# Kernel tuning notes

Measured on AMD Instinct MI355X. Metric: run time of the kernel, lower is better.

## Reference

```python
import jax, jax.numpy as jnp
import numpy as np

B, P, G = 16, 16000, 256          # images, RPN proposals, gt boxes per image
S = 512                           # batch_size_per_image
POS_FRAC = 0.25
FG_T, BG_T = 0.5, 0.5             # fg/bg IoU thresholds
NUM_CLASSES = 91
BOX_W = jnp.array([10.0, 10.0, 5.0, 5.0], jnp.float32)  # box_coder weights
BETA = 1.0 / 9.0                  # smooth_l1 beta


def _make_boxes(k, n, img=800.0, maxwh=200.0):
    k1, k2 = jax.random.split(k)
    xy = jax.random.uniform(k1, (B, n, 2)) * img
    wh = jax.random.uniform(k2, (B, n, 2)) * maxwh + 1.0
    return jnp.concatenate([xy, xy + wh], -1)


def setup_inputs() -> dict:
    key = jax.random.key(0)
    ks = jax.random.split(key, 6)
    proposals = _make_boxes(ks[0], P)
    gt_boxes = _make_boxes(ks[1], G)
    gt_labels = jax.random.randint(ks[2], (B, G), 1, NUM_CLASSES)
    gt_thetas = jax.random.uniform(ks[3], (B, G)) * np.pi
    class_logits = jax.random.normal(ks[4], (B * S, NUM_CLASSES))
    box_regression = jax.random.normal(ks[5], (B * S, NUM_CLASSES * 5))
    return dict(class_logits=class_logits, box_regression=box_regression,
                proposals=proposals, gt_boxes=gt_boxes,
                gt_thetas=gt_thetas, gt_labels=gt_labels)


def _box_iou(a, b):
    # a: [G,4] gt, b: [M,4] proposals -> [G,M]
    area_a = (a[:, 2] - a[:, 0]) * (a[:, 3] - a[:, 1])
    area_b = (b[:, 2] - b[:, 0]) * (b[:, 3] - b[:, 1])
    lt = jnp.maximum(a[:, None, :2], b[None, :, :2])
    rb = jnp.minimum(a[:, None, 2:], b[None, :, 2:])
    wh = jnp.clip(rb - lt, 0.0)
    inter = wh[..., 0] * wh[..., 1]
    return inter / (area_a[:, None] + area_b[None, :] - inter)


def _encode(ref, prop):
    pw = prop[:, 2] - prop[:, 0]; ph = prop[:, 3] - prop[:, 1]
    px = prop[:, 0] + 0.5 * pw;   py = prop[:, 1] + 0.5 * ph
    gw = ref[:, 2] - ref[:, 0];   gh = ref[:, 3] - ref[:, 1]
    gx = ref[:, 0] + 0.5 * gw;    gy = ref[:, 1] + 0.5 * gh
    t = jnp.stack([(gx - px) / pw, (gy - py) / ph,
                   jnp.log(gw / pw), jnp.log(gh / ph)], 1)
    return t * BOX_W[None, :]


def _select_training_samples(props, gtb, gtl, gtt):
    # add_gt_proposals
    props_all = jnp.concatenate([props, gtb], 0)        # [P+G,4]
    # assign_targets_to_proposals (Matcher, allow_low_quality=False)
    iou = _box_iou(gtb, props_all)                      # [G,P+G]
    vals = iou.max(0)
    matches = iou.argmax(0)                             # clamped matched idxs
    below = vals < BG_T
    between = (vals >= BG_T) & (vals < FG_T)
    lbl = gtl[matches]
    lbl = jnp.where(below, 0, lbl)      # background
    lbl = jnp.where(between, -1, lbl)   # ignored
    # BalancedPositiveNegativeSampler (deterministic first-k variant)
    pos = lbl > 0
    neg = lbl == 0
    n_pos = jnp.minimum(pos.sum(), int(S * POS_FRAC))
    sel_pos = pos & (jnp.cumsum(pos) <= n_pos)
    sel_neg = neg & (jnp.cumsum(neg) <= (S - n_pos))
    mask = sel_pos | sel_neg
    sampled = jnp.argsort((~mask).astype(jnp.int32), stable=True)[:S]  # sorted selected idxs
    props_s = props_all[sampled]
    lbl_s = lbl[sampled]
    m = matches[sampled]
    reg = _encode(gtb[m], props_s)                       # [S,4]
    reg_t = jnp.concatenate([reg, gtt[m][:, None]], 1)   # append theta -> [S,5]
    return lbl_s, reg_t


def _fastrcnn_loss(class_logits, box_regression, labels, reg_targets):
    N = class_logits.shape[0]
    logp = jax.nn.log_softmax(class_logits, -1)
    cls_loss = -jnp.take_along_axis(logp, labels[:, None], 1).mean()
    br = box_regression.reshape(N, -1, 5)
    idx = jnp.broadcast_to(labels[:, None, None], (N, 1, 5))
    pred = jnp.take_along_axis(br, idx, axis=1)[:, 0, :]
    d = pred - reg_targets
    ad = jnp.abs(d)
    sl1 = jnp.where(ad < BETA, 0.5 * d * d / BETA, ad - 0.5 * BETA)
    pos = (labels > 0).astype(sl1.dtype)
    box_loss = jnp.sum(sl1 * pos[:, None]) / N
    return jnp.stack([cls_loss, box_loss])


def reference(class_logits, box_regression, proposals, gt_boxes, gt_thetas, gt_labels):
    labels, reg_t = jax.vmap(_select_training_samples)(proposals, gt_boxes, gt_labels, gt_thetas)
    labels = labels.reshape(-1)
    reg_t = reg_t.reshape(-1, 5)
    return _fastrcnn_loss(class_logits, box_regression, labels, reg_t)
```

## Files before the change

kernel.cpp:

```cpp
#include <hip/hip_runtime.h>

#define NB 16
#define NP 16000
#define NG 256
#define NM (NP + NG)
#define NSTRIP 254
#define NS 512
#define NCLS 91
#define SL1_BETA (1.0f/9.0f)
#define LOSS_BLOCKS 512

__global__ __launch_bounds__(256) void match_kernel(
    const float4* __restrict__ props4,
    const float4* __restrict__ gt4,
    const int*    __restrict__ gt_labels,
    unsigned long long* __restrict__ posmask,
    unsigned int* __restrict__ posinfo)
{
    __shared__ float4   gbox[NG];
    __shared__ float    gar[NG];
    __shared__ int      glab[NG];
    __shared__ unsigned qm[256][9];

    const int b   = blockIdx.y;
    const int tid = threadIdx.x;

    {
        const float4 v = gt4[(size_t)b * NG + tid];
        gbox[tid] = v;
        gar[tid]  = (v.z - v.x) * (v.w - v.y);
        glab[tid] = gt_labels[b * NG + tid];
    }
    __syncthreads();

    const int j = blockIdx.x * 256 + tid;
    if (j >= NM) return;

    if (j >= NP) {
        int g = j - NP;
        posinfo[(size_t)b * NM + j] = ((unsigned)g << 16) | (unsigned)glab[g];
        if ((tid & 63) == 0) posmask[b * NSTRIP + (j >> 6)] = ~0ull;
        return;
    }

    const float4 p  = props4[(size_t)b * NP + j];
    const float  ap = (p.z - p.x) * (p.w - p.y);

    int qcnt = 0, gfirst = 0;
    for (int w = 0; w < 8; ++w) {
        unsigned m = 0;
        #pragma unroll
        for (int t = 0; t < 32; ++t) {
            const int g = w * 32 + t;
            const float4 gb = gbox[g];
            const float  ga = gar[g];
            float lx = fmaxf(gb.x, p.x), ly = fmaxf(gb.y, p.y);
            float rx = fminf(gb.z, p.z), ry = fminf(gb.w, p.w);
            float ww = fmaxf(rx - lx, 0.0f), hh = fmaxf(ry - ly, 0.0f);
            float inter = ww * hh;
            float tt = ga + ap;
            if (fmaf(inter, 3.0f, -tt) >= 0.0f) m |= (1u << t);
        }
        qm[tid][w] = m;
        if (qcnt == 0 && m) gfirst = w * 32 + (__ffs(m) - 1);
        qcnt += __popc(m);
    }

    const bool pos = qcnt > 0;
    unsigned long long word = __ballot(pos);
    if ((tid & 63) == 0) posmask[b * NSTRIP + (j >> 6)] = word;

    if (pos) {
        int gstar = gfirst;
        if (qcnt > 1) {
            float ib = -1.0f, ub = 1.0f; gstar = 0;
            for (int w = 0; w < 8; ++w) {
                unsigned m = qm[tid][w];
                while (m) {
                    int t = __ffs(m) - 1; m &= m - 1;
                    int g = w * 32 + t;
                    const float4 gb = gbox[g];
                    float lx = fmaxf(gb.x, p.x), ly = fmaxf(gb.y, p.y);
                    float rx = fminf(gb.z, p.z), ry = fminf(gb.w, p.w);
                    float ww = fmaxf(rx - lx, 0.0f), hh = fmaxf(ry - ly, 0.0f);
                    float inter = ww * hh;
                    float u = (gar[g] + ap) - inter;
                    if (inter * ub > ib * u) { ib = inter; ub = u; gstar = g; }
                }
            }
        }
        posinfo[(size_t)b * NM + j] = ((unsigned)gstar << 16) | (unsigned)glab[gstar];
    }
}

__global__ __launch_bounds__(256) void sample_kernel(
    const float4* __restrict__ props4,
    const float4* __restrict__ gt4,
    const float*  __restrict__ gt_thetas,
    const unsigned long long* __restrict__ posmask,
    const unsigned int* __restrict__ posinfo,
    int*   __restrict__ labels_out,
    float* __restrict__ regt_out)
{
    __shared__ int sampled[NS];
    __shared__ int wsum[4];

    const int b    = blockIdx.x;
    const int tid  = threadIdx.x;
    const int lane = tid & 63;
    const int wid  = tid >> 6;

    unsigned long long pm = 0ull, nm = 0ull;
    if (tid < NSTRIP) { pm = posmask[b * NSTRIP + tid]; nm = ~pm; }
    int cp = __popcll(pm), cn = __popcll(nm);
    int val  = (cp << 16) | cn;
    int incl = val;
    #pragma unroll
    for (int off = 1; off < 64; off <<= 1) {
        int u = __shfl_up(incl, off, 64);
        if (lane >= off) incl += u;
    }
    if (lane == 63) wsum[wid] = incl;
    __syncthreads();
    int wbase = 0;
    #pragma unroll
    for (int w = 0; w < 4; ++w) if (w < wid) wbase += wsum[w];
    int tot  = wsum[0] + wsum[1] + wsum[2] + wsum[3];
    int excl = wbase + incl - val;
    int rp = excl >> 16, rn = excl & 0xffff;
    int posT = tot >> 16, negT = tot & 0xffff;
    int np = posT < 128 ? posT : 128;
    int nn = NS - np; if (nn > negT) nn = negT;

    const int base = tid * 64;
    if (tid < NSTRIP) {
        #pragma unroll 4
        for (int e = 0; e < 64; ++e) {
            int idx = base + e;
            if ((pm >> e) & 1ull) {
                if (rp < np) sampled[rp + (rn < nn ? rn : nn)] = idx;
                rp++;
            } else {
                if (rn < nn) sampled[rn + (rp < np ? rp : np)] = idx;
                rn++;
            }
        }
    }
    __syncthreads();
    if (tid == 0 && np + nn < NS) {
        int cpp = 0, cnn = 0, i = np + nn;
        for (int idx = 0; idx < NM && i < NS; ++idx) {
            unsigned long long w = posmask[b * NSTRIP + (idx >> 6)];
            bool p = (w >> (idx & 63)) & 1ull;
            bool sel;
            if (p) { sel = cpp < np; cpp++; } else { sel = cnn < nn; cnn++; }
            if (!sel) sampled[i++] = idx;
        }
    }
    __syncthreads();

    for (int i = tid; i < NS; i += 256) {
        int idx = sampled[i];
        unsigned long long w = posmask[b * NSTRIP + (idx >> 6)];
        bool pos = (w >> (idx & 63)) & 1ull;
        int lbl = 0;
        if (pos) {
            unsigned info = posinfo[(size_t)b * NM + idx];
            int m = info >> 16; lbl = info & 0xffff;
            float4 pv = (idx < NP) ? props4[(size_t)b * NP + idx]
                                   : gt4[(size_t)b * NG + (idx - NP)];
            float4 rv = gt4[(size_t)b * NG + m];
            float pw = pv.z - pv.x, ph = pv.w - pv.y;
            float px = pv.x + 0.5f * pw, py = pv.y + 0.5f * ph;
            float gw = rv.z - rv.x, gh = rv.w - rv.y;
            float gx = rv.x + 0.5f * gw, gy = rv.y + 0.5f * gh;
            float* o = regt_out + ((size_t)b * NS + i) * 5;
            o[0] = 10.0f * (gx - px) / pw;
            o[1] = 10.0f * (gy - py) / ph;
            o[2] = 5.0f * logf(gw / pw);
            o[3] = 5.0f * logf(gh / ph);
            o[4] = gt_thetas[b * NG + m];
        }
        labels_out[b * NS + i] = lbl;
    }
}

__global__ __launch_bounds__(256) void loss_kernel(
    const float* __restrict__ logits,
    const float* __restrict__ boxreg,
    const int*   __restrict__ labels,
    const float* __restrict__ regt,
    float2* __restrict__ partials)
{
    const int wave  = threadIdx.x >> 6;
    const int lane  = threadIdx.x & 63;
    const int gwave = blockIdx.x * 4 + wave;
    const int NWAVE = LOSS_BLOCKS * 4;
    const int N     = NB * NS;

    float cls_acc = 0.0f, box_acc = 0.0f;

    for (int r = gwave; r < N; r += NWAVE) {
        const float* row = logits + (size_t)r * NCLS;
        float a = (lane < NCLS)      ? row[lane]      : -3.0e38f;
        float c = (lane + 64 < NCLS) ? row[lane + 64] : -3.0e38f;
        float mx = fmaxf(a, c);
        #pragma unroll
        for (int o = 32; o; o >>= 1) mx = fmaxf(mx, __shfl_xor(mx, o, 64));
        float ssum = 0.0f;
        if (lane < NCLS)      ssum += expf(a - mx);
        if (lane + 64 < NCLS) ssum += expf(c - mx);
        #pragma unroll
        for (int o = 32; o; o >>= 1) ssum += __shfl_xor(ssum, o, 64);

        int lab = labels[r];
        float xl = (lab < 64) ? __shfl(a, lab, 64) : __shfl(c, lab - 64, 64);
        if (lane == 0) cls_acc += -(xl - mx - logf(ssum));

        if (lab > 0) {
            float d = 0.0f;
            if (lane < 5) {
                float pv = boxreg[(size_t)r * (NCLS * 5) + lab * 5 + lane];
                float tv = regt[(size_t)r * 5 + lane];
                d = pv - tv;
            }
            float ad = fabsf(d);
            float sl = (ad < SL1_BETA) ? 0.5f * d * d / SL1_BETA : ad - 0.5f * SL1_BETA;
            sl += __shfl_xor(sl, 4, 8);
            sl += __shfl_xor(sl, 2, 8);
            sl += __shfl_xor(sl, 1, 8);
            if (lane == 0) box_acc += sl;
        }
    }

    __shared__ float cpart[4], bpart[4];
    if (lane == 0) { cpart[wave] = cls_acc; bpart[wave] = box_acc; }
    __syncthreads();
    if (threadIdx.x == 0) {
        partials[blockIdx.x] = make_float2(cpart[0] + cpart[1] + cpart[2] + cpart[3],
                                           bpart[0] + bpart[1] + bpart[2] + bpart[3]);
    }
}

__global__ void final_kernel(const float2* __restrict__ partials,
                             float* __restrict__ out)
{
    const int tid  = threadIdx.x;
    const int lane = tid & 63;
    const int wid  = tid >> 6;
    float2 v0 = partials[tid];
    float2 v1 = partials[tid + 256];
    float c = v0.x + v1.x, bx = v0.y + v1.y;
    #pragma unroll
    for (int o = 32; o; o >>= 1) {
        c  += __shfl_xor(c, o, 64);
        bx += __shfl_xor(bx, o, 64);
    }
    __shared__ float cc[4], bb[4];
    if (lane == 0) { cc[wid] = c; bb[wid] = bx; }
    __syncthreads();
    if (tid == 0) {
        const float invN = 1.0f / (float)(NB * NS);
        out[0] = (cc[0] + cc[1] + cc[2] + cc[3]) * invN;
        out[1] = (bb[0] + bb[1] + bb[2] + bb[3]) * invN;
    }
}

extern "C" void kernel_launch(void* const* d_in, const int* in_sizes, int n_in,
                              void* d_out, int out_size, void* d_ws, size_t ws_size,
                              hipStream_t stream)
{
    const float* class_logits   = (const float*)d_in[0];
    const float* box_regression = (const float*)d_in[1];
    const float4* props4        = (const float4*)d_in[2];
    const float4* gt4           = (const float4*)d_in[3];
    const float* gt_thetas      = (const float*)d_in[4];
    const int*   gt_labels      = (const int*)d_in[5];
    float* out = (float*)d_out;

    char* ws = (char*)d_ws;
    unsigned long long* posmask = (unsigned long long*)ws;
    unsigned int* posinfo = (unsigned int*)(ws + ((size_t)NB * NSTRIP * 8 + 255 & ~255ull));
    float2* partials = (float2*)((char*)posinfo + ((size_t)NB * NM * 4 + 255 & ~255ull));
    int* labs   = (int*)((char*)partials + (LOSS_BLOCKS * sizeof(float2) + 255 & ~255ull));
    float* regt = (float*)(labs + (size_t)NB * NS);

    hipLaunchKernelGGL(match_kernel, dim3(64, NB), dim3(256), 0, stream,
                       props4, gt4, gt_labels, posmask, posinfo);
    hipLaunchKernelGGL(sample_kernel, dim3(NB), dim3(256), 0, stream,
                       props4, gt4, gt_thetas, posmask, posinfo, labs, regt);
    hipLaunchKernelGGL(loss_kernel, dim3(LOSS_BLOCKS), dim3(256), 0, stream,
                       class_logits, box_regression, labs, regt, partials);
    hipLaunchKernelGGL(final_kernel, dim3(1), dim3(256), 0, stream, partials, out);
}
```

Before: 55.56 us.

## Process two proposals per thread in match kernel and fuse final reduction

```diff
diff --git a/kernel.cpp b/kernel.cpp
--- a/kernel.cpp
+++ b/kernel.cpp
@@ -15,15 +15,17 @@
     const float4* __restrict__ gt4,
     const int*    __restrict__ gt_labels,
     unsigned long long* __restrict__ posmask,
-    unsigned int* __restrict__ posinfo)
+    unsigned int* __restrict__ posinfo,
+    unsigned int* __restrict__ cnt)
 {
     __shared__ float4   gbox[NG];
     __shared__ float    gar[NG];
     __shared__ int      glab[NG];
-    __shared__ unsigned qm[256][9];
+    __shared__ unsigned qm[256][17];
 
     const int b   = blockIdx.y;
     const int tid = threadIdx.x;
+    if (b == 0 && blockIdx.x == 0 && tid == 0) *cnt = 0;
 
     {
         const float4 v = gt4[(size_t)b * NG + tid];
@@ -33,49 +35,74 @@
     }
     __syncthreads();
 
-    const int j = blockIdx.x * 256 + tid;
-    if (j >= NM) return;
-
-    if (j >= NP) {
-        int g = j - NP;
-        posinfo[(size_t)b * NM + j] = ((unsigned)g << 16) | (unsigned)glab[g];
-        if ((tid & 63) == 0) posmask[b * NSTRIP + (j >> 6)] = ~0ull;
-        return;
-    }
-
-    const float4 p  = props4[(size_t)b * NP + j];
-    const float  ap = (p.z - p.x) * (p.w - p.y);
-
-    int qcnt = 0, gfirst = 0;
+    const int jA = blockIdx.x * 512 + tid;
+    const int jB = jA + 256;
+    const bool haveB = (jB < NM);
+
+    const float4 pA = (jA < NP) ? props4[(size_t)b * NP + jA]
+                                : gt4[(size_t)b * NG + (jA - NP)];
+    float4 pB = make_float4(0.f, 0.f, 0.f, 0.f);
+    if (haveB) pB = (jB < NP) ? props4[(size_t)b * NP + jB]
+                              : gt4[(size_t)b * NG + (jB - NP)];
+    const float apA = (pA.z - pA.x) * (pA.w - pA.y);
+    const float apB = (pB.z - pB.x) * (pB.w - pB.y);
+
+    int qcA = 0, qcB = 0, gfA = 0, gfB = 0;
     for (int w = 0; w < 8; ++w) {
-        unsigned m = 0;
+        unsigned mA = 0, mB = 0;
         #pragma unroll
         for (int t = 0; t < 32; ++t) {
             const int g = w * 32 + t;
             const float4 gb = gbox[g];
             const float  ga = gar[g];
-            float lx = fmaxf(gb.x, p.x), ly = fmaxf(gb.y, p.y);
-            float rx = fminf(gb.z, p.z), ry = fminf(gb.w, p.w);
-            float ww = fmaxf(rx - lx, 0.0f), hh = fmaxf(ry - ly, 0.0f);
-            float inter = ww * hh;
-            float tt = ga + ap;
-            if (fmaf(inter, 3.0f, -tt) >= 0.0f) m |= (1u << t);
-        }
-        qm[tid][w] = m;
-        if (qcnt == 0 && m) gfirst = w * 32 + (__ffs(m) - 1);
-        qcnt += __popc(m);
-    }
-
-    const bool pos = qcnt > 0;
-    unsigned long long word = __ballot(pos);
-    if ((tid & 63) == 0) posmask[b * NSTRIP + (j >> 6)] = word;
-
-    if (pos) {
-        int gstar = gfirst;
-        if (qcnt > 1) {
+            {
+                float lx = fmaxf(gb.x, pA.x), ly = fmaxf(gb.y, pA.y);
+                float rx = fminf(gb.z, pA.z), ry = fminf(gb.w, pA.w);
+                float ww = fmaxf(rx - lx, 0.0f), hh = fmaxf(ry - ly, 0.0f);
+                float inter = ww * hh;
+                float tt = ga + apA;
+                if (fmaf(inter, 3.0f, -tt) >= 0.0f) mA |= (1u << t);
+            }
+            {
+                float lx = fmaxf(gb.x, pB.x), ly = fmaxf(gb.y, pB.y);
+                float rx = fminf(gb.z, pB.z), ry = fminf(gb.w, pB.w);
+                float ww = fmaxf(rx - lx, 0.0f), hh = fmaxf(ry - ly, 0.0f);
+                float inter = ww * hh;
+                float tt = ga + apB;
+                if (fmaf(inter, 3.0f, -tt) >= 0.0f) mB |= (1u << t);
+            }
+        }
+        qm[tid][w]     = mA;
+        qm[tid][8 + w] = mB;
+        if (qcA == 0 && mA) gfA = w * 32 + (__ffs(mA) - 1);
+        if (qcB == 0 && mB) gfB = w * 32 + (__ffs(mB) - 1);
+        qcA += __popc(mA);
+        qcB += __popc(mB);
+    }
+
+    const int lane0 = ((tid & 63) == 0);
+    {
+        unsigned long long wordA = __ballot(qcA > 0);
+        if (lane0) posmask[b * NSTRIP + (jA >> 6)] = wordA;
+    }
+    if (haveB) {
+        unsigned long long wordB = __ballot(qcB > 0);
+        if (lane0) posmask[b * NSTRIP + (jB >> 6)] = wordB;
+    }
+
+    #pragma unroll
+    for (int side = 0; side < 2; ++side) {
+        const int   qc = side ? qcB : qcA;
+        if (qc == 0) continue;
+        if (side && !haveB) continue;
+        const int    j   = side ? jB : jA;
+        const float4 p   = side ? pB : pA;
+        const float  ap  = side ? apB : apA;
+        int gstar        = side ? gfB : gfA;
+        if (qc > 1) {
             float ib = -1.0f, ub = 1.0f; gstar = 0;
             for (int w = 0; w < 8; ++w) {
-                unsigned m = qm[tid][w];
+                unsigned m = qm[tid][side * 8 + w];
                 while (m) {
                     int t = __ffs(m) - 1; m &= m - 1;
                     int g = w * 32 + t;
@@ -190,7 +217,9 @@
     const float* __restrict__ boxreg,
     const int*   __restrict__ labels,
     const float* __restrict__ regt,
-    float2* __restrict__ partials)
+    float2* __restrict__ partials,
+    unsigned int* __restrict__ cnt,
+    float* __restrict__ out)
 {
     const int wave  = threadIdx.x >> 6;
     const int lane  = threadIdx.x & 63;
@@ -234,35 +263,37 @@
     }
 
     __shared__ float cpart[4], bpart[4];
+    __shared__ int amLast;
     if (lane == 0) { cpart[wave] = cls_acc; bpart[wave] = box_acc; }
     __syncthreads();
     if (threadIdx.x == 0) {
         partials[blockIdx.x] = make_float2(cpart[0] + cpart[1] + cpart[2] + cpart[3],
                                            bpart[0] + bpart[1] + bpart[2] + bpart[3]);
-    }
-}
-
-__global__ void final_kernel(const float2* __restrict__ partials,
-                             float* __restrict__ out)
-{
-    const int tid  = threadIdx.x;
-    const int lane = tid & 63;
-    const int wid  = tid >> 6;
-    float2 v0 = partials[tid];
-    float2 v1 = partials[tid + 256];
-    float c = v0.x + v1.x, bx = v0.y + v1.y;
-    #pragma unroll
-    for (int o = 32; o; o >>= 1) {
-        c  += __shfl_xor(c, o, 64);
-        bx += __shfl_xor(bx, o, 64);
-    }
-    __shared__ float cc[4], bb[4];
-    if (lane == 0) { cc[wid] = c; bb[wid] = bx; }
-    __syncthreads();
-    if (tid == 0) {
-        const float invN = 1.0f / (float)(NB * NS);
-        out[0] = (cc[0] + cc[1] + cc[2] + cc[3]) * invN;
-        out[1] = (bb[0] + bb[1] + bb[2] + bb[3]) * invN;
+        __threadfence();
+        amLast = (atomicAdd(cnt, 1u) == LOSS_BLOCKS - 1);
+    }
+    __syncthreads();
+
+    if (amLast) {
+        __threadfence();
+        const int tid = threadIdx.x;
+        const int wid = tid >> 6;
+        float2 v0 = partials[tid];
+        float2 v1 = partials[tid + 256];
+        float c = v0.x + v1.x, bx = v0.y + v1.y;
+        #pragma unroll
+        for (int o = 32; o; o >>= 1) {
+            c  += __shfl_xor(c, o, 64);
+            bx += __shfl_xor(bx, o, 64);
+        }
+        __shared__ float cc[4], bb[4];
+        if (lane == 0) { cc[wid] = c; bb[wid] = bx; }
+        __syncthreads();
+        if (tid == 0) {
+            const float invN = 1.0f / (float)(NB * NS);
+            out[0] = (cc[0] + cc[1] + cc[2] + cc[3]) * invN;
+            out[1] = (bb[0] + bb[1] + bb[2] + bb[3]) * invN;
+        }
     }
 }
 
@@ -282,14 +313,14 @@
     unsigned long long* posmask = (unsigned long long*)ws;
     unsigned int* posinfo = (unsigned int*)(ws + ((size_t)NB * NSTRIP * 8 + 255 & ~255ull));
     float2* partials = (float2*)((char*)posinfo + ((size_t)NB * NM * 4 + 255 & ~255ull));
-    int* labs   = (int*)((char*)partials + (LOSS_BLOCKS * sizeof(float2) + 255 & ~255ull));
+    unsigned int* cnt = (unsigned int*)((char*)partials + ((LOSS_BLOCKS * sizeof(float2) + 255) & ~255ull));
+    int* labs   = (int*)((char*)cnt + 256);
     float* regt = (float*)(labs + (size_t)NB * NS);
 
-    hipLaunchKernelGGL(match_kernel, dim3(64, NB), dim3(256), 0, stream,
-                       props4, gt4, gt_labels, posmask, posinfo);
+    hipLaunchKernelGGL(match_kernel, dim3(32, NB), dim3(256), 0, stream,
+                       props4, gt4, gt_labels, posmask, posinfo, cnt);
     hipLaunchKernelGGL(sample_kernel, dim3(NB), dim3(256), 0, stream,
                        props4, gt4, gt_thetas, posmask, posinfo, labs, regt);
     hipLaunchKernelGGL(loss_kernel, dim3(LOSS_BLOCKS), dim3(256), 0, stream,
-                       class_logits, box_regression, labs, regt, partials);
-    hipLaunchKernelGGL(final_kernel, dim3(1), dim3(256), 0, stream, partials, out);
+                       class_logits, box_regression, labs, regt, partials, cnt, out);
 }
```

New measurement: 61.01 us. 1.1x slower.

## Split each proposal's GT scan across two lanes and drop posmask buffer

Applied to the files above, without the earlier changes.

```diff
diff --git a/kernel.cpp b/kernel.cpp
--- a/kernel.cpp
+++ b/kernel.cpp
@@ -14,13 +14,12 @@
     const float4* __restrict__ props4,
     const float4* __restrict__ gt4,
     const int*    __restrict__ gt_labels,
-    unsigned long long* __restrict__ posmask,
     unsigned int* __restrict__ posinfo)
 {
     __shared__ float4   gbox[NG];
     __shared__ float    gar[NG];
     __shared__ int      glab[NG];
-    __shared__ unsigned qm[256][9];
+    __shared__ unsigned qst[256][5];
 
     const int b   = blockIdx.y;
     const int tid = threadIdx.x;
@@ -33,63 +32,82 @@
     }
     __syncthreads();
 
-    const int j = blockIdx.x * 256 + tid;
-    if (j >= NM) return;
-
-    if (j >= NP) {
-        int g = j - NP;
-        posinfo[(size_t)b * NM + j] = ((unsigned)g << 16) | (unsigned)glab[g];
-        if ((tid & 63) == 0) posmask[b * NSTRIP + (j >> 6)] = ~0ull;
-        return;
-    }
-
-    const float4 p  = props4[(size_t)b * NP + j];
-    const float  ap = (p.z - p.x) * (p.w - p.y);
-
-    int qcnt = 0, gfirst = 0;
-    for (int w = 0; w < 8; ++w) {
+    const int h     = tid & 1;
+    const int p     = tid >> 1;
+    const int j     = blockIdx.x * 128 + p;
+    const int gbase = h * 128;
+
+    const float4 pb = (j < NP) ? props4[(size_t)b * NP + j]
+                               : gt4[(size_t)b * NG + (j - NP)];
+    const float ap = (pb.z - pb.x) * (pb.w - pb.y);
+
+    int qcnt = 0, gf = -1;
+    for (int w = 0; w < 4; ++w) {
         unsigned m = 0;
         #pragma unroll
         for (int t = 0; t < 32; ++t) {
-            const int g = w * 32 + t;
+            const int g = gbase + w * 32 + t;
             const float4 gb = gbox[g];
             const float  ga = gar[g];
-            float lx = fmaxf(gb.x, p.x), ly = fmaxf(gb.y, p.y);
-            float rx = fminf(gb.z, p.z), ry = fminf(gb.w, p.w);
+            float lx = fmaxf(gb.x, pb.x), ly = fmaxf(gb.y, pb.y);
+            float rx = fminf(gb.z, pb.z), ry = fminf(gb.w, pb.w);
             float ww = fmaxf(rx - lx, 0.0f), hh = fmaxf(ry - ly, 0.0f);
             float inter = ww * hh;
             float tt = ga + ap;
             if (fmaf(inter, 3.0f, -tt) >= 0.0f) m |= (1u << t);
         }
-        qm[tid][w] = m;
-        if (qcnt == 0 && m) gfirst = w * 32 + (__ffs(m) - 1);
+        qst[tid][w] = m;
+        if (qcnt == 0 && m) gf = w * 32 + (__ffs(m) - 1);
         qcnt += __popc(m);
     }
 
-    const bool pos = qcnt > 0;
-    unsigned long long word = __ballot(pos);
-    if ((tid & 63) == 0) posmask[b * NSTRIP + (j >> 6)] = word;
-
-    if (pos) {
-        int gstar = gfirst;
-        if (qcnt > 1) {
-            float ib = -1.0f, ub = 1.0f; gstar = 0;
-            for (int w = 0; w < 8; ++w) {
-                unsigned m = qm[tid][w];
-                while (m) {
-                    int t = __ffs(m) - 1; m &= m - 1;
-                    int g = w * 32 + t;
-                    const float4 gb = gbox[g];
-                    float lx = fmaxf(gb.x, p.x), ly = fmaxf(gb.y, p.y);
-                    float rx = fminf(gb.z, p.z), ry = fminf(gb.w, p.w);
-                    float ww = fmaxf(rx - lx, 0.0f), hh = fmaxf(ry - ly, 0.0f);
-                    float inter = ww * hh;
-                    float u = (gar[g] + ap) - inter;
-                    if (inter * ub > ib * u) { ib = inter; ub = u; gstar = g; }
-                }
+    float ib = -1.0f, ub = 1.0f;
+    int   gstar = -1;
+    if (qcnt == 1) {
+        const int g = gbase + gf;
+        const float4 gb = gbox[g];
+        float lx = fmaxf(gb.x, pb.x), ly = fmaxf(gb.y, pb.y);
+        float rx = fminf(gb.z, pb.z), ry = fminf(gb.w, pb.w);
+        float ww = fmaxf(rx - lx, 0.0f), hh = fmaxf(ry - ly, 0.0f);
+        ib = ww * hh;
+        ub = (gar[g] + ap) - ib;
+        gstar = g;
+    } else if (qcnt > 1) {
+        for (int w = 0; w < 4; ++w) {
+            unsigned m = qst[tid][w];
+            while (m) {
+                int t = __ffs(m) - 1; m &= m - 1;
+                int g = gbase + w * 32 + t;
+                const float4 gb = gbox[g];
+                float lx = fmaxf(gb.x, pb.x), ly = fmaxf(gb.y, pb.y);
+                float rx = fminf(gb.z, pb.z), ry = fminf(gb.w, pb.w);
+                float ww = fmaxf(rx - lx, 0.0f), hh = fmaxf(ry - ly, 0.0f);
+                float inter = ww * hh;
+                float u = (gar[g] + ap) - inter;
+                if (inter * ub > ib * u) { ib = inter; ub = u; gstar = g; }
             }
         }
-        posinfo[(size_t)b * NM + j] = ((unsigned)gstar << 16) | (unsigned)glab[gstar];
+    }
+
+    const int   oq  = __shfl_xor(qcnt, 1, 64);
+    const float oib = __shfl_xor(ib, 1, 64);
+    const float oub = __shfl_xor(ub, 1, 64);
+    const int   og  = __shfl_xor(gstar, 1, 64);
+    const int qtot = qcnt + oq;
+    int gm;
+    if (qcnt > 0 && oq > 0) {
+        bool otherWins;
+        if (h == 0) otherWins = (oib * ub > ib * oub);
+        else        otherWins = !(ib * oub > oib * ub);
+        gm = otherWins ? og : gstar;
+    } else {
+        gm = (qcnt > 0) ? gstar : og;
+    }
+
+    if (h == 0) {
+        unsigned info = 0;
+        if (qtot > 0) info = ((unsigned)gm << 16) | (unsigned)glab[gm];
+        posinfo[(size_t)b * NM + j] = info;
     }
 }
 
@@ -97,7 +115,6 @@
     const float4* __restrict__ props4,
     const float4* __restrict__ gt4,
     const float*  __restrict__ gt_thetas,
-    const unsigned long long* __restrict__ posmask,
     const unsigned int* __restrict__ posinfo,
     int*   __restrict__ labels_out,
     float* __restrict__ regt_out)
@@ -109,10 +126,25 @@
     const int tid  = threadIdx.x;
     const int lane = tid & 63;
     const int wid  = tid >> 6;
-
-    unsigned long long pm = 0ull, nm = 0ull;
-    if (tid < NSTRIP) { pm = posmask[b * NSTRIP + tid]; nm = ~pm; }
-    int cp = __popcll(pm), cn = __popcll(nm);
+    const unsigned* P = posinfo + (size_t)b * NM;
+    const int base = tid * 64;
+
+    unsigned long long pm = 0ull;
+    int cn = 0;
+    if (tid < NSTRIP) {
+        const uint4* Pv = reinterpret_cast<const uint4*>(P + base);
+        #pragma unroll
+        for (int q = 0; q < 16; ++q) {
+            uint4 v = Pv[q];
+            int e = q * 4;
+            if (v.x) pm |= 1ull << (e + 0);
+            if (v.y) pm |= 1ull << (e + 1);
+            if (v.z) pm |= 1ull << (e + 2);
+            if (v.w) pm |= 1ull << (e + 3);
+        }
+        cn = 64 - __popcll(pm);
+    }
+    int cp = (tid < NSTRIP) ? __popcll(pm) : 0;
     int val  = (cp << 16) | cn;
     int incl = val;
     #pragma unroll
@@ -132,7 +164,6 @@
     int np = posT < 128 ? posT : 128;
     int nn = NS - np; if (nn > negT) nn = negT;
 
-    const int base = tid * 64;
     if (tid < NSTRIP) {
         #pragma unroll 4
         for (int e = 0; e < 64; ++e) {
@@ -150,8 +181,7 @@
     if (tid == 0 && np + nn < NS) {
         int cpp = 0, cnn = 0, i = np + nn;
         for (int idx = 0; idx < NM && i < NS; ++idx) {
-            unsigned long long w = posmask[b * NSTRIP + (idx >> 6)];
-            bool p = (w >> (idx & 63)) & 1ull;
+            bool p = P[idx] != 0;
             bool sel;
             if (p) { sel = cpp < np; cpp++; } else { sel = cnn < nn; cnn++; }
             if (!sel) sampled[i++] = idx;
@@ -161,11 +191,9 @@
 
     for (int i = tid; i < NS; i += 256) {
         int idx = sampled[i];
-        unsigned long long w = posmask[b * NSTRIP + (idx >> 6)];
-        bool pos = (w >> (idx & 63)) & 1ull;
+        unsigned info = P[idx];
         int lbl = 0;
-        if (pos) {
-            unsigned info = posinfo[(size_t)b * NM + idx];
+        if (info) {
             int m = info >> 16; lbl = info & 0xffff;
             float4 pv = (idx < NP) ? props4[(size_t)b * NP + idx]
                                    : gt4[(size_t)b * NG + (idx - NP)];
@@ -279,16 +307,15 @@
     float* out = (float*)d_out;
 
     char* ws = (char*)d_ws;
-    unsigned long long* posmask = (unsigned long long*)ws;
-    unsigned int* posinfo = (unsigned int*)(ws + ((size_t)NB * NSTRIP * 8 + 255 & ~255ull));
-    float2* partials = (float2*)((char*)posinfo + ((size_t)NB * NM * 4 + 255 & ~255ull));
-    int* labs   = (int*)((char*)partials + (LOSS_BLOCKS * sizeof(float2) + 255 & ~255ull));
+    unsigned int* posinfo = (unsigned int*)ws;
+    float2* partials = (float2*)(ws + (((size_t)NB * NM * 4 + 255) & ~255ull));
+    int* labs   = (int*)((char*)partials + ((LOSS_BLOCKS * sizeof(float2) + 255) & ~255ull));
     float* regt = (float*)(labs + (size_t)NB * NS);
 
-    hipLaunchKernelGGL(match_kernel, dim3(64, NB), dim3(256), 0, stream,
-                       props4, gt4, gt_labels, posmask, posinfo);
+    hipLaunchKernelGGL(match_kernel, dim3(127, NB), dim3(256), 0, stream,
+                       props4, gt4, gt_labels, posinfo);
     hipLaunchKernelGGL(sample_kernel, dim3(NB), dim3(256), 0, stream,
-                       props4, gt4, gt_thetas, posmask, posinfo, labs, regt);
+                       props4, gt4, gt_thetas, posinfo, labs, regt);
     hipLaunchKernelGGL(loss_kernel, dim3(LOSS_BLOCKS), dim3(256), 0, stream,
                        class_logits, box_regression, labs, regt, partials);
     hipLaunchKernelGGL(final_kernel, dim3(1), dim3(256), 0, stream, partials, out);
```

Result: no change. 54.69 us (-1.6%).
